# Performance work log

Measured on AMD Instinct MI355X. Metric: run time of the kernel, lower is better.

The kernel has to match this reference:

```python
import jax, jax.numpy as jnp
import numpy as np
import math

D_MODEL = 1024
MEM_SIZE = 4096
N_HEADS = 8
BATCH = 4
SEQ = 1024
TOP_K = min(SEQ, MEM_SIZE // 10)  # 409, matches torch: min(seq_len, memory_size//10)
UPDATE_RATE = 0.01


def _gelu(x):
    return jax.nn.gelu(x, approximate=False)  # torch nn.GELU default (erf)


def setup_inputs() -> dict:
    key = jax.random.key(0)
    ks = jax.random.split(key, 26)
    w = lambda k, shape, s=0.02: (jax.random.normal(k, shape, jnp.float32) * s)
    inp = {
        "x": jax.random.normal(ks[0], (BATCH, SEQ, D_MODEL), jnp.float32),
        "memory_bank": jax.random.normal(ks[1], (MEM_SIZE, D_MODEL), jnp.float32) * 0.1,
        "memory_indices": jax.random.randint(ks[2], (BATCH, TOP_K), 0, MEM_SIZE, jnp.int32),
        # memory_encoder: Linear -> GELU -> Linear
        "enc_w1": w(ks[3], (D_MODEL, D_MODEL)), "enc_b1": jnp.zeros((D_MODEL,), jnp.float32),
        "enc_w2": w(ks[4], (D_MODEL, D_MODEL)), "enc_b2": jnp.zeros((D_MODEL,), jnp.float32),
        # MultiheadAttention in/out projections
        "wq": w(ks[5], (D_MODEL, D_MODEL)), "bq": jnp.zeros((D_MODEL,), jnp.float32),
        "wk": w(ks[6], (D_MODEL, D_MODEL)), "bk": jnp.zeros((D_MODEL,), jnp.float32),
        "wv": w(ks[7], (D_MODEL, D_MODEL)), "bv": jnp.zeros((D_MODEL,), jnp.float32),
        "wo": w(ks[8], (D_MODEL, D_MODEL)), "bo": jnp.zeros((D_MODEL,), jnp.float32),
        # memory_decoder: Linear -> GELU -> Linear
        "dec_w1": w(ks[9], (D_MODEL, D_MODEL)), "dec_b1": jnp.zeros((D_MODEL,), jnp.float32),
        "dec_w2": w(ks[10], (D_MODEL, D_MODEL)), "dec_b2": jnp.zeros((D_MODEL,), jnp.float32),
        # LayerNorm
        "ln_g": jnp.ones((D_MODEL,), jnp.float32), "ln_b": jnp.zeros((D_MODEL,), jnp.float32),
        # importance_scorer: Linear(d,64) -> GELU -> Linear(64,1) -> Sigmoid
        "imp_w1": w(ks[11], (D_MODEL, 64)), "imp_b1": jnp.zeros((64,), jnp.float32),
        "imp_w2": w(ks[12], (64, 1)), "imp_b2": jnp.zeros((1,), jnp.float32),
    }
    return inp


def reference(x, memory_bank, memory_indices,
              enc_w1, enc_b1, enc_w2, enc_b2,
              wq, bq, wk, bk, wv, bv, wo, bo,
              dec_w1, dec_b1, dec_w2, dec_b2,
              ln_g, ln_b, imp_w1, imp_b1, imp_w2, imp_b2):
    B, L, D = x.shape
    M = memory_bank.shape[0]
    H = N_HEADS
    dh = D // H

    # memory_encoder (dropout inactive at eval)
    enc = _gelu(x @ enc_w1 + enc_b1) @ enc_w2 + enc_b2  # [B,L,D]

    # cross-attention: query = encoded input, key/value = memory bank (shared across batch)
    q = (enc @ wq + bq).reshape(B, L, H, dh)
    k = (memory_bank @ wk + bk).reshape(M, H, dh)
    v = (memory_bank @ wv + bv).reshape(M, H, dh)
    scores = jnp.einsum('blhd,mhd->bhlm', q, k) * (1.0 / math.sqrt(dh))
    attn = jax.nn.softmax(scores, axis=-1)                 # [B,H,L,M]
    ctx = jnp.einsum('bhlm,mhd->blhd', attn, v).reshape(B, L, D)
    mem_out = ctx @ wo + bo

    # memory_decoder + residual + LayerNorm
    dec = _gelu(mem_out @ dec_w1 + dec_b1) @ dec_w2 + dec_b2
    comb = x + dec
    mu = jnp.mean(comb, axis=-1, keepdims=True)
    var = jnp.var(comb, axis=-1, keepdims=True)
    out = (comb - mu) / jnp.sqrt(var + 1e-5) * ln_g + ln_b  # [B,L,D]

    # _update_memory: importance top-k select + sequential EMA scatter into memory bank
    imp = jax.nn.sigmoid(_gelu(x @ imp_w1 + imp_b1) @ imp_w2 + imp_b2)[..., 0]  # [B,L]
    _, top_idx = jax.lax.top_k(imp, TOP_K)                  # [B,K]
    top_tok = jnp.take_along_axis(x, top_idx[..., None], axis=1)  # [B,K,D]

    # faithful to the torch double loop (b outer, k inner): sequential EMA with
    # chained updates on index collisions
    flat_idx = memory_indices.reshape(-1)
    flat_tok = top_tok.reshape(-1, D)

    def body(mem, xs):
        i, t = xs
        row = (1.0 - UPDATE_RATE) * mem[i] + UPDATE_RATE * t
        return mem.at[i].set(row), None

    new_mem, _ = jax.lax.scan(body, memory_bank, (flat_idx, flat_tok))
    return out, new_mem
```

## Files before the change

### kernel.cpp

```cpp
#include <hip/hip_runtime.h>

typedef unsigned short u16;
typedef __attribute__((ext_vector_type(4))) int i4;
typedef __attribute__((ext_vector_type(4))) unsigned u4;
typedef __attribute__((ext_vector_type(4))) unsigned short us4;
typedef __attribute__((ext_vector_type(8))) short short8;
typedef __attribute__((ext_vector_type(4))) float f4;

#define D_MODEL 1024
#define ROWS 4096
#define NHEAD 8
#define DH 128
#define TOPK 409
#define NUPD 1636
#define NBATCH 4
#define MAXC 64
#define ATTNROWS 32768

__device__ __forceinline__ u16 f2bf(float f) {
  unsigned u = __builtin_bit_cast(unsigned, f);
  u += 0x7fffu + ((u >> 16) & 1u);
  return (u16)(u >> 16);
}
__device__ __forceinline__ float bf2f(u16 b) {
  unsigned u = ((unsigned)b) << 16;
  return __builtin_bit_cast(float, u);
}
__device__ __forceinline__ float gelu_f(float v) {
  return 0.5f * v * (1.0f + erff(v * 0.70710678118654752f));
}
__device__ __forceinline__ void gload16(const void* g, void* l) {
  __builtin_amdgcn_global_load_lds((const __attribute__((address_space(1))) void*)g,
                                   (__attribute__((address_space(3))) void*)l, 16, 0, 0);
}

__global__ __launch_bounds__(256) void conv_kernel(const float* __restrict__ in,
                                                   u16* __restrict__ out, int n4) {
  int i = blockIdx.x * 256 + threadIdx.x;
  if (i < n4) {
    f4 v = ((const f4*)in)[i];
    us4 o;
    o.x = f2bf(v.x); o.y = f2bf(v.y); o.z = f2bf(v.z); o.w = f2bf(v.w);
    ((us4*)out)[i] = o;
  }
}

__global__ __launch_bounds__(256) void wtrans8_kernel(const float* s0, const float* s1,
                                                      const float* s2, const float* s3,
                                                      const float* s4, const float* s5,
                                                      const float* s6, const float* s7,
                                                      u16* __restrict__ dst) {
  const float* srcs[8] = {s0, s1, s2, s3, s4, s5, s6, s7};
  const float* w = srcs[blockIdx.z];
  u16* wt = dst + (size_t)blockIdx.z * (1024 * 1024);
  __shared__ float t[32][33];
  int tx = threadIdx.x & 31, ty = threadIdx.x >> 5;
  int k0 = blockIdx.y * 32, n0 = blockIdx.x * 32;
  for (int r = 0; r < 4; ++r)
    t[ty + r * 8][tx] = w[(size_t)(k0 + ty + r * 8) * 1024 + n0 + tx];
  __syncthreads();
  for (int r = 0; r < 4; ++r)
    wt[(size_t)(n0 + ty + r * 8) * 1024 + k0 + tx] = f2bf(t[tx][ty + r * 8]);
}

template <int EPI>
__global__ __launch_bounds__(256) void gemm_bt(const u16* __restrict__ A,
                                               const u16* __restrict__ BT,
                                               const float* __restrict__ bias,
                                               void* __restrict__ C) {
  __shared__ __align__(16) char al[2 * 128 * 64];
  __shared__ __align__(16) char bl[2 * 64 * 64];
  const int K = 1024, N = 1024;
  const int id = blockIdx.x;
  const int xcd = id & 7, j = id >> 3;
  const int m0 = ((j & 3) * 8 + xcd) * 128;
  const int n0 = (j >> 2) * 64;
  const int tid = threadIdx.x;
  const int lane = tid & 63, wid = tid >> 6;
  const int g = lane >> 4, qi = lane & 15;
  const int wr = wid >> 1, wc = wid & 1;
  f4 acc[4][2] = {};

  const int a0r = tid >> 2, a0b = (tid & 3) ^ ((a0r >> 1) & 3);
  const int c1 = tid + 256;
  const int a1r = c1 >> 2, a1b = (c1 & 3) ^ ((a1r >> 1) & 3);
  const int b0r = tid >> 2, b0b = (tid & 3) ^ ((b0r >> 1) & 3);

#define STAGE(buf, kt)                                                                   \
  {                                                                                      \
    const int k0_ = (kt) * 32;                                                           \
    gload16(A + (size_t)(m0 + a0r) * K + k0_ + a0b * 8, al + (buf) * 8192 + tid * 16);   \
    gload16(A + (size_t)(m0 + a1r) * K + k0_ + a1b * 8, al + (buf) * 8192 + c1 * 16);    \
    gload16(BT + (size_t)(n0 + b0r) * K + k0_ + b0b * 8, bl + (buf) * 4096 + tid * 16);  \
  }

  STAGE(0, 0);
  __syncthreads();
  int cur = 0;
  for (int kt = 0; kt < 32; ++kt) {
    if (kt + 1 < 32) STAGE(cur ^ 1, kt + 1);
    short8 af[4], bfr[2];
    for (int i = 0; i < 4; ++i) {
      int r = wr * 64 + i * 16 + qi;
      af[i] = *(const short8*)(al + cur * 8192 + r * 64 + ((g ^ ((r >> 1) & 3))) * 16);
    }
    for (int sn = 0; sn < 2; ++sn) {
      int r = wc * 32 + sn * 16 + qi;
      bfr[sn] = *(const short8*)(bl + cur * 4096 + r * 64 + ((g ^ ((r >> 1) & 3))) * 16);
    }
    for (int i = 0; i < 4; ++i)
      for (int sn = 0; sn < 2; ++sn)
        acc[i][sn] = __builtin_amdgcn_mfma_f32_16x16x32_bf16(af[i], bfr[sn], acc[i][sn], 0, 0, 0);
    __syncthreads();
    cur ^= 1;
  }
#undef STAGE

  for (int i = 0; i < 4; ++i) {
    int row = m0 + wr * 64 + i * 16 + g * 4;
    for (int sn = 0; sn < 2; ++sn) {
      int col = n0 + wc * 32 + sn * 16 + qi;
      float bv = bias[col];
      for (int jj = 0; jj < 4; ++jj) {
        float v = acc[i][sn][jj] + bv;
        if constexpr (EPI == 1) v = gelu_f(v);
        if constexpr (EPI == 2)
          ((float*)C)[(size_t)(row + jj) * N + col] = v;
        else
          ((u16*)C)[(size_t)(row + jj) * N + col] = f2bf(v);
      }
    }
  }
}

__global__ __launch_bounds__(256) void gemm_kv(const u16* __restrict__ A,
                                               const u16* __restrict__ BT,
                                               const float* __restrict__ bk,
                                               const float* __restrict__ bv,
                                               u16* __restrict__ Ck, u16* __restrict__ CvT) {
  __shared__ __align__(16) char pool[2 * 128 * 64 + 2 * 64 * 64];
  char* al = pool;
  char* bl = pool + 2 * 128 * 64;
  const int id = blockIdx.x;
  const int xcd = id & 7, j = id >> 3;
  const int m0 = ((j & 3) * 8 + xcd) * 128;
  const int n0 = (j >> 2) * 64;
  const int tid = threadIdx.x;
  const int lane = tid & 63, wid = tid >> 6;
  const int g = lane >> 4, qi = lane & 15;
  const int wr = wid >> 1, wc = wid & 1;
  const int K = 1024, M = 4096;
  f4 acc[4][2] = {};

  const int a0r = tid >> 2, a0b = (tid & 3) ^ ((a0r >> 1) & 3);
  const int c1 = tid + 256;
  const int a1r = c1 >> 2, a1b = (c1 & 3) ^ ((a1r >> 1) & 3);
  const int b0r = tid >> 2, b0b = (tid & 3) ^ ((b0r >> 1) & 3);

#define STAGE(buf, kt)                                                                   \
  {                                                                                      \
    const int k0_ = (kt) * 32;                                                           \
    gload16(A + (size_t)(m0 + a0r) * K + k0_ + a0b * 8, al + (buf) * 8192 + tid * 16);   \
    gload16(A + (size_t)(m0 + a1r) * K + k0_ + a1b * 8, al + (buf) * 8192 + c1 * 16);    \
    gload16(BT + (size_t)(n0 + b0r) * K + k0_ + b0b * 8, bl + (buf) * 4096 + tid * 16);  \
  }

  STAGE(0, 0);
  __syncthreads();
  int cur = 0;
  for (int kt = 0; kt < 32; ++kt) {
    if (kt + 1 < 32) STAGE(cur ^ 1, kt + 1);
    short8 af[4], bfr[2];
    for (int i = 0; i < 4; ++i) {
      int r = wr * 64 + i * 16 + qi;
      af[i] = *(const short8*)(al + cur * 8192 + r * 64 + ((g ^ ((r >> 1) & 3))) * 16);
    }
    for (int sn = 0; sn < 2; ++sn) {
      int r = wc * 32 + sn * 16 + qi;
      bfr[sn] = *(const short8*)(bl + cur * 4096 + r * 64 + ((g ^ ((r >> 1) & 3))) * 16);
    }
    for (int i = 0; i < 4; ++i)
      for (int sn = 0; sn < 2; ++sn)
        acc[i][sn] = __builtin_amdgcn_mfma_f32_16x16x32_bf16(af[i], bfr[sn], acc[i][sn], 0, 0, 0);
    __syncthreads();
    cur ^= 1;
  }
#undef STAGE

  if (n0 < 1024) {
    for (int i = 0; i < 4; ++i) {
      int row = m0 + wr * 64 + i * 16 + g * 4;
      for (int sn = 0; sn < 2; ++sn) {
        int col = n0 + wc * 32 + sn * 16 + qi;
        float bvv = bk[col];
        for (int jj = 0; jj < 4; ++jj)
          Ck[(size_t)(row + jj) * 1024 + col] = f2bf(acc[i][sn][jj] + bvv);
      }
    }
  } else {
    u16(*t)[132] = (u16(*)[132])pool;
    __syncthreads();
    for (int i = 0; i < 4; ++i)
      for (int sn = 0; sn < 2; ++sn) {
        int nl = wc * 32 + sn * 16 + qi;
        float bvv = bv[n0 - 1024 + nl];
        for (int jj = 0; jj < 4; ++jj)
          t[nl][wr * 64 + i * 16 + g * 4 + jj] = f2bf(acc[i][sn][jj] + bvv);
      }
    __syncthreads();
    int r = tid >> 2, cg = tid & 3;
    for (int v = 0; v < 4; ++v) {
      us4 val = *(const us4*)&t[r][cg * 32 + v * 8];
      *(us4*)&CvT[(size_t)(n0 - 1024 + r) * M + m0 + cg * 32 + v * 8] = val;
    }
  }
}

template <int LP>
__global__ __launch_bounds__(512) void attn_kernel(const u16* __restrict__ q,
                                                   const u16* __restrict__ kp,
                                                   const u16* __restrict__ vT,
                                                   u16* __restrict__ cp0, u16* __restrict__ cp1,
                                                   u16* __restrict__ cp2, u16* __restrict__ cp3,
                                                   float* __restrict__ ml) {
  constexpr int MR = 4096 >> LP;
  constexpr int NT = MR / 64;
  __shared__ __align__(16) char kl[64 * 256];
  __shared__ __align__(16) char vl[128 * 128];
  const int id = blockIdx.x;
  const int h = id & 7;
  const int rest = id >> 3;
  const int part = rest & ((1 << LP) - 1);
  const int qblk = (rest >> LP) & 7;
  const int b = rest >> (3 + LP);
  const int tid = threadIdx.x;
  const int lane = tid & 63, wid = tid >> 6;
  const int g = lane >> 4, qi = lane & 15;
  const int qrow = b * 1024 + qblk * 128 + wid * 16 + qi;
  const float scale = 0.08838834764831845f;
  u16* ctp = (part == 0) ? cp0 : (part == 1) ? cp1 : (part == 2) ? cp2 : cp3;

  short8 qf[4];
  for (int kk = 0; kk < 4; ++kk)
    qf[kk] = *(const short8*)(q + (size_t)qrow * 1024 + h * 128 + kk * 32 + g * 8);

  const int kc0 = tid, kc1 = tid + 512;
  const int kr0 = kc0 >> 4, kb0 = kc0 & 15, kr1 = kc1 >> 4, kb1 = kc1 & 15;
  const int vr0 = kc0 >> 3, vb0 = kc0 & 7, vr1 = kc1 >> 3, vb1 = kc1 & 7;
  const int kd0 = kr0 * 256 + (kb0 ^ (kr0 & 7)) * 16;
  const int kd1 = kr1 * 256 + (kb1 ^ (kr1 & 7)) * 16;
  const int vd0 = vr0 * 128 + (vb0 ^ (vr0 & 7)) * 16;
  const int vd1 = vr1 * 128 + (vb1 ^ (vr1 & 7)) * 16;
  const int mbase = part * MR;
  const u16* kg0 = kp + (size_t)kr0 * 1024 + h * 128 + kb0 * 8;
  const u16* kg1 = kp + (size_t)kr1 * 1024 + h * 128 + kb1 * 8;
  const u16* vg0 = vT + (size_t)(h * 128 + vr0) * 4096 + vb0 * 8;
  const u16* vg1 = vT + (size_t)(h * 128 + vr1) * 4096 + vb1 * 8;

  i4 kreg0, kreg1, vreg0, vreg1;
#define LOADREGS(mt_)                                  \
  {                                                    \
    const int m0_ = mbase + (mt_) * 64;                \
    kreg0 = *(const i4*)(kg0 + (size_t)m0_ * 1024);    \
    kreg1 = *(const i4*)(kg1 + (size_t)m0_ * 1024);    \
    vreg0 = *(const i4*)(vg0 + m0_);                   \
    vreg1 = *(const i4*)(vg1 + m0_);                   \
  }

  f4 ct[8] = {};
  float mrun = -1e30f, lsum = 0.0f;

  LOADREGS(0);
  for (int mt = 0; mt < NT; ++mt) {
    __syncthreads();
    *(i4*)(kl + kd0) = kreg0;
    *(i4*)(kl + kd1) = kreg1;
    *(i4*)(vl + vd0) = vreg0;
    *(i4*)(vl + vd1) = vreg1;
    __syncthreads();
    if (mt + 1 < NT) LOADREGS(mt + 1);

    f4 st[4] = {};
    for (int s = 0; s < 4; ++s) {
      int n = s * 16 + qi;
      const char* krow = kl + n * 256;
      int sw = n & 7;
      for (int kk = 0; kk < 4; ++kk) {
        short8 a = *(const short8*)(krow + ((kk * 4 + g) ^ sw) * 16);
        st[s] = __builtin_amdgcn_mfma_f32_16x16x32_bf16(a, qf[kk], st[s], 0, 0, 0);
      }
    }
    float sv[16];
    float tmax = -1e30f;
    for (int s = 0; s < 4; ++s)
      for (int jj = 0; jj < 4; ++jj) {
        float v = st[s][jj] * scale;
        sv[s * 4 + jj] = v;
        tmax = fmaxf(tmax, v);
      }
    tmax = fmaxf(tmax, __shfl_xor(tmax, 16, 64));
    tmax = fmaxf(tmax, __shfl_xor(tmax, 32, 64));
    float mnew = fmaxf(mrun, tmax);
    float r = __expf(mrun - mnew);
    float psum = 0.0f;
    for (int i = 0; i < 16; ++i) {
      sv[i] = __expf(sv[i] - mnew);
      psum += sv[i];
    }
    psum += __shfl_xor(psum, 16, 64);
    psum += __shfl_xor(psum, 32, 64);
    lsum = lsum * r + psum;
    mrun = mnew;
    for (int i = 0; i < 8; ++i) ct[i] = ct[i] * r;

    unsigned pk0[4], pk1[4];
    for (int s = 0; s < 4; ++s) {
      pk0[s] = (unsigned)f2bf(sv[s * 4 + 0]) | ((unsigned)f2bf(sv[s * 4 + 1]) << 16);
      pk1[s] = (unsigned)f2bf(sv[s * 4 + 2]) | ((unsigned)f2bf(sv[s * 4 + 3]) << 16);
    }
    const int src1 = qi + ((g & 1) << 5);
    const int src2 = src1 + 16;
    const bool hi = (g & 2) != 0;
    for (int p = 0; p < 2; ++p) {
      unsigned a0 = __shfl(pk0[2 * p], src1, 64), b0 = __shfl(pk0[2 * p + 1], src1, 64);
      unsigned a1 = __shfl(pk1[2 * p], src1, 64), b1 = __shfl(pk1[2 * p + 1], src1, 64);
      unsigned a2 = __shfl(pk0[2 * p], src2, 64), b2 = __shfl(pk0[2 * p + 1], src2, 64);
      unsigned a3 = __shfl(pk1[2 * p], src2, 64), b3 = __shfl(pk1[2 * p + 1], src2, 64);
      u4 bw;
      bw.x = hi ? b0 : a0; bw.y = hi ? b1 : a1; bw.z = hi ? b2 : a2; bw.w = hi ? b3 : a3;
      short8 pf = __builtin_bit_cast(short8, bw);
      for (int d = 0; d < 8; ++d) {
        int dr = d * 16 + qi;
        short8 a = *(const short8*)(vl + dr * 128 + (((p * 4 + g) ^ (dr & 7))) * 16);
        ct[d] = __builtin_amdgcn_mfma_f32_16x16x32_bf16(a, pf, ct[d], 0, 0, 0);
      }
    }
  }
#undef LOADREGS

  const int orow = ((b * 8 + h) << 10) + qblk * 128 + wid * 16 + qi;
  if (g == 0) {
    ml[(size_t)(part * ATTNROWS + orow) * 2 + 0] = mrun;
    ml[(size_t)(part * ATTNROWS + orow) * 2 + 1] = lsum;
  }
  for (int d = 0; d < 8; ++d) {
    us4 o;
    o.x = f2bf(ct[d][0]); o.y = f2bf(ct[d][1]);
    o.z = f2bf(ct[d][2]); o.w = f2bf(ct[d][3]);
    *(us4*)(ctp + (size_t)orow * 128 + d * 16 + g * 4) = o;
  }
}

__global__ __launch_bounds__(256) void combine4_kernel(const u16* __restrict__ cp0,
                                                       const u16* __restrict__ cp1,
                                                       const u16* __restrict__ cp2,
                                                       const u16* __restrict__ cp3,
                                                       const float* __restrict__ ml,
                                                       u16* __restrict__ ctx) {
  int tid = threadIdx.x;
  int row = blockIdx.x * 16 + (tid >> 4);
  int dp = (tid & 15) * 8;
  float m0 = ml[(size_t)row * 2], l0 = ml[(size_t)row * 2 + 1];
  float m1 = ml[((size_t)ATTNROWS + row) * 2], l1 = ml[((size_t)ATTNROWS + row) * 2 + 1];
  float m2 = ml[((size_t)2 * ATTNROWS + row) * 2], l2 = ml[((size_t)2 * ATTNROWS + row) * 2 + 1];
  float m3 = ml[((size_t)3 * ATTNROWS + row) * 2], l3 = ml[((size_t)3 * ATTNROWS + row) * 2 + 1];
  float m = fmaxf(fmaxf(m0, m1), fmaxf(m2, m3));
  float s0 = __expf(m0 - m), s1 = __expf(m1 - m), s2 = __expf(m2 - m), s3 = __expf(m3 - m);
  float inv = 1.0f / (l0 * s0 + l1 * s1 + l2 * s2 + l3 * s3);
  short8 c0 = *(const short8*)(cp0 + (size_t)row * 128 + dp);
  short8 c1 = *(const short8*)(cp1 + (size_t)row * 128 + dp);
  short8 c2 = *(const short8*)(cp2 + (size_t)row * 128 + dp);
  short8 c3 = *(const short8*)(cp3 + (size_t)row * 128 + dp);
  us4 o[2];
  for (int i = 0; i < 8; ++i) {
    float f = (bf2f((u16)c0[i]) * s0 + bf2f((u16)c1[i]) * s1 + bf2f((u16)c2[i]) * s2 +
               bf2f((u16)c3[i]) * s3) * inv;
    ((u16*)o)[i] = f2bf(f);
  }
  int bb = row >> 13, hh = (row >> 10) & 7, qr = row & 1023;
  *(short8*)(ctx + (size_t)((bb << 10) + qr) * 1024 + hh * 128 + dp) =
      __builtin_bit_cast(short8, o);
}

__global__ __launch_bounds__(256) void ln_kernel(const float* __restrict__ x,
                                                 const float* __restrict__ dec,
                                                 const float* __restrict__ gw,
                                                 const float* __restrict__ bw,
                                                 float* __restrict__ out,
                                                 int* __restrict__ cnt) {
  __shared__ float rs[256], rs2[256];
  int row = blockIdx.x, tid = threadIdx.x;
  if (tid == 0) cnt[row] = 0;
  float c[4];
  float s = 0.0f, s2 = 0.0f;
  for (int i = 0; i < 4; ++i) {
    int col = tid + i * 256;
    float v = x[(size_t)row * 1024 + col] + dec[(size_t)row * 1024 + col];
    c[i] = v; s += v; s2 += v * v;
  }
  rs[tid] = s; rs2[tid] = s2;
  __syncthreads();
  for (int st = 128; st > 0; st >>= 1) {
    if (tid < st) { rs[tid] += rs[tid + st]; rs2[tid] += rs2[tid + st]; }
    __syncthreads();
  }
  float mu = rs[0] * (1.0f / 1024.0f);
  float var = rs2[0] * (1.0f / 1024.0f) - mu * mu;
  float inv = rsqrtf(var + 1e-5f);
  for (int i = 0; i < 4; ++i) {
    int col = tid + i * 256;
    out[(size_t)row * 1024 + col] = (c[i] - mu) * inv * gw[col] + bw[col];
  }
}

__global__ __launch_bounds__(256) void imp_kernel(const float* __restrict__ x,
                                                  const float* __restrict__ w1,
                                                  const float* __restrict__ b1,
                                                  const float* __restrict__ w2,
                                                  const float* __restrict__ b2,
                                                  float* __restrict__ imp) {
  __shared__ float xs[8][1024];
  int tid = threadIdx.x;
  int lane = tid & 63, wid = tid >> 6;
  size_t base = (size_t)blockIdx.x * 8192;
  for (int i = 0; i < 32; ++i) ((float*)xs)[tid + i * 256] = x[base + tid + i * 256];
  __syncthreads();
  int r0 = wid * 2, r1 = wid * 2 + 1;
  float a0 = 0.0f, a1 = 0.0f;
  for (int k = 0; k < 1024; ++k) {
    float wv = w1[k * 64 + lane];
    a0 += xs[r0][k] * wv;
    a1 += xs[r1][k] * wv;
  }
  float h0 = gelu_f(a0 + b1[lane]) * w2[lane];
  float h1 = gelu_f(a1 + b1[lane]) * w2[lane];
  for (int d = 1; d < 64; d <<= 1) {
    h0 += __shfl_xor(h0, d, 64);
    h1 += __shfl_xor(h1, d, 64);
  }
  if (lane == 0) {
    imp[blockIdx.x * 8 + r0] = 1.0f / (1.0f + expf(-(h0 + b2[0])));
    imp[blockIdx.x * 8 + r1] = 1.0f / (1.0f + expf(-(h1 + b2[0])));
  }
}

__global__ __launch_bounds__(512) void topk_kernel(const float* __restrict__ imp,
                                                   int* __restrict__ tidx) {
  __shared__ float v[1024];
  __shared__ int ix[1024];
  int b = blockIdx.x, tid = threadIdx.x;
  for (int i = tid; i < 1024; i += 512) { v[i] = imp[b * 1024 + i]; ix[i] = i; }
  __syncthreads();
  for (int k = 2; k <= 1024; k <<= 1) {
    for (int j = k >> 1; j > 0; j >>= 1) {
      for (int t = tid; t < 1024; t += 512) {
        int p = t ^ j;
        if (p > t) {
          float va = v[t], vb = v[p];
          int ia = ix[t], ib = ix[p];
          bool ord = (va > vb) || (va == vb && ia < ib);
          bool up = ((t & k) == 0);
          if (up ? !ord : ord) { v[t] = vb; v[p] = va; ix[t] = ib; ix[p] = ia; }
        }
      }
      __syncthreads();
    }
  }
  for (int t = tid; t < TOPK; t += 512) tidx[b * TOPK + t] = ix[t];
}

__global__ __launch_bounds__(128) void rank_kernel(const int* __restrict__ midx,
                                                   int* __restrict__ cnt,
                                                   int* __restrict__ slot) {
  __shared__ int mi[NUPD];
  int tid = threadIdx.x;
  for (int i = tid; i < NUPD; i += 128) mi[i] = midx[i];
  __syncthreads();
  int j = blockIdx.x * 128 + tid;
  if (j < NUPD) {
    int r = mi[j], rank = 0;
    for (int jp = 0; jp < j; ++jp) rank += (mi[jp] == r) ? 1 : 0;
    if (rank < MAXC) slot[r * MAXC + rank] = j;
    atomicAdd(&cnt[r], 1);
  }
}

__global__ __launch_bounds__(256) void apply_kernel(const float* __restrict__ x,
                                                    const float* __restrict__ mem,
                                                    const int* __restrict__ tidx,
                                                    const int* __restrict__ cnt,
                                                    const int* __restrict__ slot,
                                                    float* __restrict__ outm) {
  int row = blockIdx.x, tid = threadIdx.x;
  f4 acc = ((const f4*)(mem + (size_t)row * 1024))[tid];
  int c = cnt[row];
  c = c < MAXC ? c : MAXC;
  for (int t = 0; t < c; ++t) {
    int j = slot[row * MAXC + t];
    int b = j / TOPK;
    int tr = tidx[j];
    f4 xv = ((const f4*)(x + ((size_t)b * 1024 + tr) * 1024))[tid];
    acc = acc * 0.99f + xv * 0.01f;
  }
  ((f4*)(outm + (size_t)row * 1024))[tid] = acc;
}

extern "C" void kernel_launch(void* const* d_in, const int* in_sizes, int n_in,
                              void* d_out, int out_size, void* d_ws, size_t ws_size,
                              hipStream_t stream) {
  const float* x = (const float*)d_in[0];
  const float* memory_bank = (const float*)d_in[1];
  const int* memory_indices = (const int*)d_in[2];
  const float* enc_w1 = (const float*)d_in[3];
  const float* enc_b1 = (const float*)d_in[4];
  const float* enc_w2 = (const float*)d_in[5];
  const float* enc_b2 = (const float*)d_in[6];
  const float* wq = (const float*)d_in[7];
  const float* bq = (const float*)d_in[8];
  const float* wk = (const float*)d_in[9];
  const float* bk = (const float*)d_in[10];
  const float* wv = (const float*)d_in[11];
  const float* bv = (const float*)d_in[12];
  const float* wo = (const float*)d_in[13];
  const float* bo = (const float*)d_in[14];
  const float* dec_w1 = (const float*)d_in[15];
  const float* dec_b1 = (const float*)d_in[16];
  const float* dec_w2 = (const float*)d_in[17];
  const float* dec_b2 = (const float*)d_in[18];
  const float* ln_g = (const float*)d_in[19];
  const float* ln_b = (const float*)d_in[20];
  const float* imp_w1 = (const float*)d_in[21];
  const float* imp_b1 = (const float*)d_in[22];
  const float* imp_w2 = (const float*)d_in[23];
  const float* imp_b2 = (const float*)d_in[24];

  char* ws = (char*)d_ws;
  u16* buf0 = (u16*)(ws);
  u16* buf1 = (u16*)(ws + (8ull << 20));
  u16* buf2 = (u16*)(ws + (16ull << 20));
  u16* buf3 = (u16*)(ws + (24ull << 20));
  u16* buf4 = (u16*)(ws + (32ull << 20));
  float* decb = (float*)(ws + (40ull << 20));
  u16* wtb = (u16*)(ws + (56ull << 20));
  float* impb = (float*)(ws + (72ull << 20));
  int* tidx = (int*)(ws + (72ull << 20) + (1 << 16));
  int* cnt = (int*)buf3;
  int* slot = (int*)(ws + (24ull << 20) + (1 << 16));
  u16* cp0 = buf0;
  u16* cp1 = buf2;
  u16* cp2 = (u16*)(ws + (40ull << 20));
  u16* cp3 = (u16*)(ws + (48ull << 20));
  float* ml = (float*)(ws + (56ull << 20));

  const int NM = 1024 * 1024;
  u16* wt_e1 = wtb + 0 * NM;
  u16* wt_e2 = wtb + 1 * NM;
  u16* wt_q = wtb + 2 * NM;
  u16* wt_k = wtb + 3 * NM;
  u16* wt_o = wtb + 5 * NM;
  u16* wt_d1 = wtb + 6 * NM;
  u16* wt_d2 = wtb + 7 * NM;

  conv_kernel<<<4096, 256, 0, stream>>>(x, buf0, ROWS * D_MODEL / 4);
  conv_kernel<<<4096, 256, 0, stream>>>(memory_bank, buf2, ROWS * D_MODEL / 4);
  wtrans8_kernel<<<dim3(32, 32, 8), 256, 0, stream>>>(enc_w1, enc_w2, wq, wk, wv, wo,
                                                      dec_w1, dec_w2, wtb);

  gemm_bt<1><<<512, 256, 0, stream>>>(buf0, wt_e1, enc_b1, buf1);
  gemm_bt<0><<<512, 256, 0, stream>>>(buf1, wt_e2, enc_b2, buf0);
  gemm_bt<0><<<512, 256, 0, stream>>>(buf0, wt_q, bq, buf1);
  gemm_kv<<<1024, 256, 0, stream>>>(buf2, wt_k, bk, bv, buf3, buf4);

  attn_kernel<2><<<1024, 512, 0, stream>>>(buf1, buf3, buf4, cp0, cp1, cp2, cp3, ml);
  combine4_kernel<<<2048, 256, 0, stream>>>(cp0, cp1, cp2, cp3, ml, buf1);

  gemm_bt<0><<<512, 256, 0, stream>>>(buf1, wt_o, bo, buf0);
  gemm_bt<1><<<512, 256, 0, stream>>>(buf0, wt_d1, dec_b1, buf2);
  gemm_bt<2><<<512, 256, 0, stream>>>(buf2, wt_d2, dec_b2, decb);
  ln_kernel<<<4096, 256, 0, stream>>>(x, decb, ln_g, ln_b, (float*)d_out, cnt);

  imp_kernel<<<512, 256, 0, stream>>>(x, imp_w1, imp_b1, imp_w2, imp_b2, impb);
  topk_kernel<<<NBATCH, 512, 0, stream>>>(impb, tidx);
  rank_kernel<<<13, 128, 0, stream>>>(memory_indices, cnt, slot);
  apply_kernel<<<4096, 256, 0, stream>>>(x, memory_bank, tidx, cnt, slot,
                                         (float*)d_out + (size_t)ROWS * D_MODEL);
}
```

Before: 442.2 us.

## Process two query tiles per wave in attention to reuse K/V fragments

```diff
diff --git a/kernel.cpp b/kernel.cpp
--- a/kernel.cpp
+++ b/kernel.cpp
@@ -217,12 +217,12 @@
 }
 
 template <int LP>
-__global__ __launch_bounds__(512) void attn_kernel(const u16* __restrict__ q,
-                                                   const u16* __restrict__ kp,
-                                                   const u16* __restrict__ vT,
-                                                   u16* __restrict__ cp0, u16* __restrict__ cp1,
-                                                   u16* __restrict__ cp2, u16* __restrict__ cp3,
-                                                   float* __restrict__ ml) {
+__global__ __launch_bounds__(256, 3) void attn_kernel(const u16* __restrict__ q,
+                                                      const u16* __restrict__ kp,
+                                                      const u16* __restrict__ vT,
+                                                      u16* __restrict__ cp0, u16* __restrict__ cp1,
+                                                      u16* __restrict__ cp2, u16* __restrict__ cp3,
+                                                      float* __restrict__ ml) {
   constexpr int MR = 4096 >> LP;
   constexpr int NT = MR / 64;
   __shared__ __align__(16) char kl[64 * 256];
@@ -236,118 +236,171 @@
   const int tid = threadIdx.x;
   const int lane = tid & 63, wid = tid >> 6;
   const int g = lane >> 4, qi = lane & 15;
-  const int qrow = b * 1024 + qblk * 128 + wid * 16 + qi;
+  const int qrow0 = b * 1024 + qblk * 128 + wid * 32 + qi;
+  const int qrow1 = qrow0 + 16;
   const float scale = 0.08838834764831845f;
   u16* ctp = (part == 0) ? cp0 : (part == 1) ? cp1 : (part == 2) ? cp2 : cp3;
 
-  short8 qf[4];
-  for (int kk = 0; kk < 4; ++kk)
-    qf[kk] = *(const short8*)(q + (size_t)qrow * 1024 + h * 128 + kk * 32 + g * 8);
-
-  const int kc0 = tid, kc1 = tid + 512;
+  short8 qf0[4], qf1[4];
+  for (int kk = 0; kk < 4; ++kk) {
+    qf0[kk] = *(const short8*)(q + (size_t)qrow0 * 1024 + h * 128 + kk * 32 + g * 8);
+    qf1[kk] = *(const short8*)(q + (size_t)qrow1 * 1024 + h * 128 + kk * 32 + g * 8);
+  }
+
+  const int kc0 = tid, kc1 = tid + 256, kc2 = tid + 512, kc3 = tid + 768;
   const int kr0 = kc0 >> 4, kb0 = kc0 & 15, kr1 = kc1 >> 4, kb1 = kc1 & 15;
+  const int kr2 = kc2 >> 4, kb2 = kc2 & 15, kr3 = kc3 >> 4, kb3 = kc3 & 15;
   const int vr0 = kc0 >> 3, vb0 = kc0 & 7, vr1 = kc1 >> 3, vb1 = kc1 & 7;
+  const int vr2 = kc2 >> 3, vb2 = kc2 & 7, vr3 = kc3 >> 3, vb3 = kc3 & 7;
   const int kd0 = kr0 * 256 + (kb0 ^ (kr0 & 7)) * 16;
   const int kd1 = kr1 * 256 + (kb1 ^ (kr1 & 7)) * 16;
+  const int kd2 = kr2 * 256 + (kb2 ^ (kr2 & 7)) * 16;
+  const int kd3 = kr3 * 256 + (kb3 ^ (kr3 & 7)) * 16;
   const int vd0 = vr0 * 128 + (vb0 ^ (vr0 & 7)) * 16;
   const int vd1 = vr1 * 128 + (vb1 ^ (vr1 & 7)) * 16;
+  const int vd2 = vr2 * 128 + (vb2 ^ (vr2 & 7)) * 16;
+  const int vd3 = vr3 * 128 + (vb3 ^ (vr3 & 7)) * 16;
   const int mbase = part * MR;
-  const u16* kg0 = kp + (size_t)kr0 * 1024 + h * 128 + kb0 * 8;
-  const u16* kg1 = kp + (size_t)kr1 * 1024 + h * 128 + kb1 * 8;
-  const u16* vg0 = vT + (size_t)(h * 128 + vr0) * 4096 + vb0 * 8;
-  const u16* vg1 = vT + (size_t)(h * 128 + vr1) * 4096 + vb1 * 8;
-
-  i4 kreg0, kreg1, vreg0, vreg1;
-#define LOADREGS(mt_)                                  \
-  {                                                    \
-    const int m0_ = mbase + (mt_) * 64;                \
-    kreg0 = *(const i4*)(kg0 + (size_t)m0_ * 1024);    \
-    kreg1 = *(const i4*)(kg1 + (size_t)m0_ * 1024);    \
-    vreg0 = *(const i4*)(vg0 + m0_);                   \
-    vreg1 = *(const i4*)(vg1 + m0_);                   \
-  }
-
-  f4 ct[8] = {};
-  float mrun = -1e30f, lsum = 0.0f;
-
-  LOADREGS(0);
+  const u16* kg0 = kp + (size_t)(mbase + kr0) * 1024 + h * 128 + kb0 * 8;
+  const u16* kg1 = kp + (size_t)(mbase + kr1) * 1024 + h * 128 + kb1 * 8;
+  const u16* kg2 = kp + (size_t)(mbase + kr2) * 1024 + h * 128 + kb2 * 8;
+  const u16* kg3 = kp + (size_t)(mbase + kr3) * 1024 + h * 128 + kb3 * 8;
+  const u16* vg0 = vT + (size_t)(h * 128 + vr0) * 4096 + mbase + vb0 * 8;
+  const u16* vg1 = vT + (size_t)(h * 128 + vr1) * 4096 + mbase + vb1 * 8;
+  const u16* vg2 = vT + (size_t)(h * 128 + vr2) * 4096 + mbase + vb2 * 8;
+  const u16* vg3 = vT + (size_t)(h * 128 + vr3) * 4096 + mbase + vb3 * 8;
+
+  i4 kreg0, kreg1, kreg2, kreg3, vreg0, vreg1, vreg2, vreg3;
+#define LOADK()                                             \
+  {                                                         \
+    kreg0 = *(const i4*)kg0; kg0 += 64 * 1024;              \
+    kreg1 = *(const i4*)kg1; kg1 += 64 * 1024;              \
+    kreg2 = *(const i4*)kg2; kg2 += 64 * 1024;              \
+    kreg3 = *(const i4*)kg3; kg3 += 64 * 1024;              \
+  }
+#define LOADV()                                             \
+  {                                                         \
+    vreg0 = *(const i4*)vg0; vg0 += 64;                     \
+    vreg1 = *(const i4*)vg1; vg1 += 64;                     \
+    vreg2 = *(const i4*)vg2; vg2 += 64;                     \
+    vreg3 = *(const i4*)vg3; vg3 += 64;                     \
+  }
+
+  f4 ct0[8] = {}, ct1[8] = {};
+  float mrun0 = -1e30f, lsum0 = 0.0f, mrun1 = -1e30f, lsum1 = 0.0f;
+
+  LOADK();
+  LOADV();
   for (int mt = 0; mt < NT; ++mt) {
     __syncthreads();
-    *(i4*)(kl + kd0) = kreg0;
-    *(i4*)(kl + kd1) = kreg1;
-    *(i4*)(vl + vd0) = vreg0;
-    *(i4*)(vl + vd1) = vreg1;
+    *(i4*)(kl + kd0) = kreg0; *(i4*)(kl + kd1) = kreg1;
+    *(i4*)(kl + kd2) = kreg2; *(i4*)(kl + kd3) = kreg3;
+    *(i4*)(vl + vd0) = vreg0; *(i4*)(vl + vd1) = vreg1;
+    *(i4*)(vl + vd2) = vreg2; *(i4*)(vl + vd3) = vreg3;
     __syncthreads();
-    if (mt + 1 < NT) LOADREGS(mt + 1);
-
-    f4 st[4] = {};
+    const bool more = (mt + 1 < NT);
+    if (more) LOADK();
+
+    f4 st0[4] = {}, st1[4] = {};
     for (int s = 0; s < 4; ++s) {
       int n = s * 16 + qi;
       const char* krow = kl + n * 256;
       int sw = n & 7;
       for (int kk = 0; kk < 4; ++kk) {
         short8 a = *(const short8*)(krow + ((kk * 4 + g) ^ sw) * 16);
-        st[s] = __builtin_amdgcn_mfma_f32_16x16x32_bf16(a, qf[kk], st[s], 0, 0, 0);
+        st0[s] = __builtin_amdgcn_mfma_f32_16x16x32_bf16(a, qf0[kk], st0[s], 0, 0, 0);
+        st1[s] = __builtin_amdgcn_mfma_f32_16x16x32_bf16(a, qf1[kk], st1[s], 0, 0, 0);
       }
     }
-    float sv[16];
-    float tmax = -1e30f;
-    for (int s = 0; s < 4; ++s)
-      for (int jj = 0; jj < 4; ++jj) {
-        float v = st[s][jj] * scale;
-        sv[s * 4 + jj] = v;
-        tmax = fmaxf(tmax, v);
-      }
-    tmax = fmaxf(tmax, __shfl_xor(tmax, 16, 64));
-    tmax = fmaxf(tmax, __shfl_xor(tmax, 32, 64));
-    float mnew = fmaxf(mrun, tmax);
-    float r = __expf(mrun - mnew);
-    float psum = 0.0f;
-    for (int i = 0; i < 16; ++i) {
-      sv[i] = __expf(sv[i] - mnew);
-      psum += sv[i];
-    }
-    psum += __shfl_xor(psum, 16, 64);
-    psum += __shfl_xor(psum, 32, 64);
-    lsum = lsum * r + psum;
-    mrun = mnew;
-    for (int i = 0; i < 8; ++i) ct[i] = ct[i] * r;
-
-    unsigned pk0[4], pk1[4];
-    for (int s = 0; s < 4; ++s) {
-      pk0[s] = (unsigned)f2bf(sv[s * 4 + 0]) | ((unsigned)f2bf(sv[s * 4 + 1]) << 16);
-      pk1[s] = (unsigned)f2bf(sv[s * 4 + 2]) | ((unsigned)f2bf(sv[s * 4 + 3]) << 16);
-    }
-    const int src1 = qi + ((g & 1) << 5);
-    const int src2 = src1 + 16;
-    const bool hi = (g & 2) != 0;
-    for (int p = 0; p < 2; ++p) {
-      unsigned a0 = __shfl(pk0[2 * p], src1, 64), b0 = __shfl(pk0[2 * p + 1], src1, 64);
-      unsigned a1 = __shfl(pk1[2 * p], src1, 64), b1 = __shfl(pk1[2 * p + 1], src1, 64);
-      unsigned a2 = __shfl(pk0[2 * p], src2, 64), b2 = __shfl(pk0[2 * p + 1], src2, 64);
-      unsigned a3 = __shfl(pk1[2 * p], src2, 64), b3 = __shfl(pk1[2 * p + 1], src2, 64);
-      u4 bw;
-      bw.x = hi ? b0 : a0; bw.y = hi ? b1 : a1; bw.z = hi ? b2 : a2; bw.w = hi ? b3 : a3;
-      short8 pf = __builtin_bit_cast(short8, bw);
-      for (int d = 0; d < 8; ++d) {
-        int dr = d * 16 + qi;
-        short8 a = *(const short8*)(vl + dr * 128 + (((p * 4 + g) ^ (dr & 7))) * 16);
-        ct[d] = __builtin_amdgcn_mfma_f32_16x16x32_bf16(a, pf, ct[d], 0, 0, 0);
-      }
-    }
-  }
-#undef LOADREGS
-
-  const int orow = ((b * 8 + h) << 10) + qblk * 128 + wid * 16 + qi;
+
+    short8 pfa0, pfb0, pfa1, pfb1;
+#define SOFTMAX_PACK(ST, MRUN, LSUM, CT, PFA, PFB)                                        \
+    {                                                                                     \
+      float sv[16];                                                                       \
+      float tmax = -1e30f;                                                                \
+      for (int s = 0; s < 4; ++s)                                                         \
+        for (int jj = 0; jj < 4; ++jj) {                                                  \
+          float v = ST[s][jj] * scale;                                                    \
+          sv[s * 4 + jj] = v;                                                             \
+          tmax = fmaxf(tmax, v);                                                          \
+        }                                                                                 \
+      tmax = fmaxf(tmax, __shfl_xor(tmax, 16, 64));                                       \
+      tmax = fmaxf(tmax, __shfl_xor(tmax, 32, 64));                                       \
+      float mnew = fmaxf(MRUN, tmax);                                                     \
+      float r = __expf(MRUN - mnew);                                                      \
+      float psum = 0.0f;                                                                  \
+      for (int i = 0; i < 16; ++i) {                                                      \
+        sv[i] = __expf(sv[i] - mnew);                                                     \
+        psum += sv[i];                                                                    \
+      }                                                                                   \
+      psum += __shfl_xor(psum, 16, 64);                                                   \
+      psum += __shfl_xor(psum, 32, 64);                                                   \
+      LSUM = LSUM * r + psum;                                                             \
+      MRUN = mnew;                                                                        \
+      for (int i = 0; i < 8; ++i) CT[i] = CT[i] * r;                                      \
+      unsigned pk0[4], pk1[4];                                                            \
+      for (int s = 0; s < 4; ++s) {                                                       \
+        pk0[s] = (unsigned)f2bf(sv[s * 4 + 0]) | ((unsigned)f2bf(sv[s * 4 + 1]) << 16);   \
+        pk1[s] = (unsigned)f2bf(sv[s * 4 + 2]) | ((unsigned)f2bf(sv[s * 4 + 3]) << 16);   \
+      }                                                                                   \
+      const int src1 = qi + ((g & 1) << 5);                                               \
+      const int src2 = src1 + 16;                                                         \
+      const bool hi = (g & 2) != 0;                                                       \
+      {                                                                                   \
+        unsigned a0 = __shfl(pk0[0], src1, 64), b0 = __shfl(pk0[1], src1, 64);            \
+        unsigned a1 = __shfl(pk1[0], src1, 64), b1 = __shfl(pk1[1], src1, 64);            \
+        unsigned a2 = __shfl(pk0[0], src2, 64), b2 = __shfl(pk0[1], src2, 64);            \
+        unsigned a3 = __shfl(pk1[0], src2, 64), b3 = __shfl(pk1[1], src2, 64);            \
+        u4 bw;                                                                            \
+        bw.x = hi ? b0 : a0; bw.y = hi ? b1 : a1; bw.z = hi ? b2 : a2; bw.w = hi ? b3 : a3;\
+        PFA = __builtin_bit_cast(short8, bw);                                             \
+      }                                                                                   \
+      {                                                                                   \
+        unsigned a0 = __shfl(pk0[2], src1, 64), b0 = __shfl(pk0[3], src1, 64);            \
+        unsigned a1 = __shfl(pk1[2], src1, 64), b1 = __shfl(pk1[3], src1, 64);            \
+        unsigned a2 = __shfl(pk0[2], src2, 64), b2 = __shfl(pk0[3], src2, 64);            \
+        unsigned a3 = __shfl(pk1[2], src2, 64), b3 = __shfl(pk1[3], src2, 64);            \
+        u4 bw;                                                                            \
+        bw.x = hi ? b0 : a0; bw.y = hi ? b1 : a1; bw.z = hi ? b2 : a2; bw.w = hi ? b3 : a3;\
+        PFB = __builtin_bit_cast(short8, bw);                                             \
+      }                                                                                   \
+    }
+    SOFTMAX_PACK(st0, mrun0, lsum0, ct0, pfa0, pfb0);
+    SOFTMAX_PACK(st1, mrun1, lsum1, ct1, pfa1, pfb1);
+#undef SOFTMAX_PACK
+
+    if (more) LOADV();
+
+    for (int d = 0; d < 8; ++d) {
+      int dr = d * 16 + qi;
+      const char* vrow = vl + dr * 128;
+      int swv = dr & 7;
+      short8 a0 = *(const short8*)(vrow + ((0 * 4 + g) ^ swv) * 16);
+      ct0[d] = __builtin_amdgcn_mfma_f32_16x16x32_bf16(a0, pfa0, ct0[d], 0, 0, 0);
+      ct1[d] = __builtin_amdgcn_mfma_f32_16x16x32_bf16(a0, pfa1, ct1[d], 0, 0, 0);
+      short8 a1 = *(const short8*)(vrow + ((1 * 4 + g) ^ swv) * 16);
+      ct0[d] = __builtin_amdgcn_mfma_f32_16x16x32_bf16(a1, pfb0, ct0[d], 0, 0, 0);
+      ct1[d] = __builtin_amdgcn_mfma_f32_16x16x32_bf16(a1, pfb1, ct1[d], 0, 0, 0);
+    }
+  }
+#undef LOADK
+#undef LOADV
+
+  const int obase = ((b * 8 + h) << 10) + qblk * 128 + wid * 32 + qi;
   if (g == 0) {
-    ml[(size_t)(part * ATTNROWS + orow) * 2 + 0] = mrun;
-    ml[(size_t)(part * ATTNROWS + orow) * 2 + 1] = lsum;
+    ml[(size_t)(part * ATTNROWS + obase) * 2 + 0] = mrun0;
+    ml[(size_t)(part * ATTNROWS + obase) * 2 + 1] = lsum0;
+    ml[(size_t)(part * ATTNROWS + obase + 16) * 2 + 0] = mrun1;
+    ml[(size_t)(part * ATTNROWS + obase + 16) * 2 + 1] = lsum1;
   }
   for (int d = 0; d < 8; ++d) {
-    us4 o;
-    o.x = f2bf(ct[d][0]); o.y = f2bf(ct[d][1]);
-    o.z = f2bf(ct[d][2]); o.w = f2bf(ct[d][3]);
-    *(us4*)(ctp + (size_t)orow * 128 + d * 16 + g * 4) = o;
+    us4 o0, o1;
+    o0.x = f2bf(ct0[d][0]); o0.y = f2bf(ct0[d][1]);
+    o0.z = f2bf(ct0[d][2]); o0.w = f2bf(ct0[d][3]);
+    o1.x = f2bf(ct1[d][0]); o1.y = f2bf(ct1[d][1]);
+    o1.z = f2bf(ct1[d][2]); o1.w = f2bf(ct1[d][3]);
+    *(us4*)(ctp + (size_t)obase * 128 + d * 16 + g * 4) = o0;
+    *(us4*)(ctp + (size_t)(obase + 16) * 128 + d * 16 + g * 4) = o1;
   }
 }
 
@@ -571,7 +624,7 @@
   gemm_bt<0><<<512, 256, 0, stream>>>(buf0, wt_q, bq, buf1);
   gemm_kv<<<1024, 256, 0, stream>>>(buf2, wt_k, bk, bv, buf3, buf4);
 
-  attn_kernel<2><<<1024, 512, 0, stream>>>(buf1, buf3, buf4, cp0, cp1, cp2, cp3, ml);
+  attn_kernel<2><<<1024, 256, 0, stream>>>(buf1, buf3, buf4, cp0, cp1, cp2, cp3, ml);
   combine4_kernel<<<2048, 256, 0, stream>>>(cp0, cp1, cp2, cp3, ml, buf1);
 
   gemm_bt<0><<<512, 256, 0, stream>>>(buf1, wt_o, bo, buf0);
```

Result: slower. 632.9 us (+43.1%).

## Fold consecutive linear layers (enc_w2·wq, wo·dec_w1) into precomputed weight products

Applied to the files above, without the earlier changes.

```diff
diff --git a/kernel.cpp b/kernel.cpp
--- a/kernel.cpp
+++ b/kernel.cpp
@@ -61,6 +61,91 @@
   __syncthreads();
   for (int r = 0; r < 4; ++r)
     wt[(size_t)(n0 + ty + r * 8) * 1024 + k0 + tx] = f2bf(t[tx][ty + r * 8]);
+}
+
+__global__ __launch_bounds__(256) void bias_prep_kernel(const float* __restrict__ b2,
+                                                        const float* __restrict__ wq,
+                                                        const float* __restrict__ bq,
+                                                        const float* __restrict__ bo,
+                                                        const float* __restrict__ dw1,
+                                                        const float* __restrict__ db1,
+                                                        float* __restrict__ bqp,
+                                                        float* __restrict__ bodp) {
+  int id = blockIdx.x;
+  int n = (id & 3) * 256 + threadIdx.x;
+  const float* bvec = (id < 4) ? b2 : bo;
+  const float* W = (id < 4) ? wq : dw1;
+  const float* badd = (id < 4) ? bq : db1;
+  float* out = (id < 4) ? bqp : bodp;
+  float s = 0.0f;
+  for (int k = 0; k < 1024; ++k) s += bvec[k] * W[(size_t)k * 1024 + n];
+  out[n] = s + badd[n];
+}
+
+__global__ __launch_bounds__(256) void gemm_sq(const u16* __restrict__ A0,
+                                               const u16* __restrict__ B0,
+                                               u16* __restrict__ C0,
+                                               const u16* __restrict__ A1,
+                                               const u16* __restrict__ B1,
+                                               u16* __restrict__ C1) {
+  __shared__ __align__(16) char al[2 * 128 * 64];
+  __shared__ __align__(16) char bl[2 * 64 * 64];
+  const int K = 1024, N = 1024;
+  const int id = blockIdx.x;
+  const int which = id >> 7, j = id & 127;
+  const u16* A = which ? A1 : A0;
+  const u16* BT = which ? B1 : B0;
+  u16* C = which ? C1 : C0;
+  const int m0 = (j >> 4) * 128, n0 = (j & 15) * 64;
+  const int tid = threadIdx.x;
+  const int lane = tid & 63, wid = tid >> 6;
+  const int g = lane >> 4, qi = lane & 15;
+  const int wr = wid >> 1, wc = wid & 1;
+  f4 acc[4][2] = {};
+
+  const int a0r = tid >> 2, a0b = (tid & 3) ^ ((a0r >> 1) & 3);
+  const int c1 = tid + 256;
+  const int a1r = c1 >> 2, a1b = (c1 & 3) ^ ((a1r >> 1) & 3);
+  const int b0r = tid >> 2, b0b = (tid & 3) ^ ((b0r >> 1) & 3);
+
+#define STAGE(buf, kt)                                                                   \
+  {                                                                                      \
+    const int k0_ = (kt) * 32;                                                           \
+    gload16(A + (size_t)(m0 + a0r) * K + k0_ + a0b * 8, al + (buf) * 8192 + tid * 16);   \
+    gload16(A + (size_t)(m0 + a1r) * K + k0_ + a1b * 8, al + (buf) * 8192 + c1 * 16);    \
+    gload16(BT + (size_t)(n0 + b0r) * K + k0_ + b0b * 8, bl + (buf) * 4096 + tid * 16);  \
+  }
+
+  STAGE(0, 0);
+  __syncthreads();
+  int cur = 0;
+  for (int kt = 0; kt < 32; ++kt) {
+    if (kt + 1 < 32) STAGE(cur ^ 1, kt + 1);
+    short8 af[4], bfr[2];
+    for (int i = 0; i < 4; ++i) {
+      int r = wr * 64 + i * 16 + qi;
+      af[i] = *(const short8*)(al + cur * 8192 + r * 64 + ((g ^ ((r >> 1) & 3))) * 16);
+    }
+    for (int sn = 0; sn < 2; ++sn) {
+      int r = wc * 32 + sn * 16 + qi;
+      bfr[sn] = *(const short8*)(bl + cur * 4096 + r * 64 + ((g ^ ((r >> 1) & 3))) * 16);
+    }
+    for (int i = 0; i < 4; ++i)
+      for (int sn = 0; sn < 2; ++sn)
+        acc[i][sn] = __builtin_amdgcn_mfma_f32_16x16x32_bf16(af[i], bfr[sn], acc[i][sn], 0, 0, 0);
+    __syncthreads();
+    cur ^= 1;
+  }
+#undef STAGE
+
+  for (int i = 0; i < 4; ++i) {
+    int row = m0 + wr * 64 + i * 16 + g * 4;
+    for (int sn = 0; sn < 2; ++sn) {
+      int col = n0 + wc * 32 + sn * 16 + qi;
+      for (int jj = 0; jj < 4; ++jj)
+        C[(size_t)(row + jj) * N + col] = f2bf(acc[i][sn][jj]);
+    }
+  }
 }
 
 template <int EPI>
@@ -544,9 +629,13 @@
   u16* wtb = (u16*)(ws + (56ull << 20));
   float* impb = (float*)(ws + (72ull << 20));
   int* tidx = (int*)(ws + (72ull << 20) + (1 << 16));
+  float* bqp = (float*)(ws + (72ull << 20) + (1 << 17));
+  float* bodp = (float*)(ws + (72ull << 20) + (1 << 17) + 4096);
   int* cnt = (int*)buf3;
   int* slot = (int*)(ws + (24ull << 20) + (1 << 16));
-  u16* cp0 = buf0;
+  u16* w2n = (u16*)(ws + (40ull << 20));
+  u16* won = (u16*)(ws + (42ull << 20));
+  u16* cp0 = buf1;
   u16* cp1 = buf2;
   u16* cp2 = (u16*)(ws + (40ull << 20));
   u16* cp3 = (u16*)(ws + (48ull << 20));
@@ -554,10 +643,10 @@
 
   const int NM = 1024 * 1024;
   u16* wt_e1 = wtb + 0 * NM;
-  u16* wt_e2 = wtb + 1 * NM;
+  u16* wt_e2q = wtb + 1 * NM;
   u16* wt_q = wtb + 2 * NM;
   u16* wt_k = wtb + 3 * NM;
-  u16* wt_o = wtb + 5 * NM;
+  u16* wt_od = wtb + 5 * NM;
   u16* wt_d1 = wtb + 6 * NM;
   u16* wt_d2 = wtb + 7 * NM;
 
@@ -565,18 +654,21 @@
   conv_kernel<<<4096, 256, 0, stream>>>(memory_bank, buf2, ROWS * D_MODEL / 4);
   wtrans8_kernel<<<dim3(32, 32, 8), 256, 0, stream>>>(enc_w1, enc_w2, wq, wk, wv, wo,
                                                       dec_w1, dec_w2, wtb);
+  conv_kernel<<<1024, 256, 0, stream>>>(enc_w2, w2n, NM / 4);
+  conv_kernel<<<1024, 256, 0, stream>>>(wo, won, NM / 4);
+
+  gemm_sq<<<256, 256, 0, stream>>>(wt_q, w2n, wt_e2q, wt_d1, won, wt_od);
+  bias_prep_kernel<<<8, 256, 0, stream>>>(enc_b2, wq, bq, bo, dec_w1, dec_b1, bqp, bodp);
 
   gemm_bt<1><<<512, 256, 0, stream>>>(buf0, wt_e1, enc_b1, buf1);
-  gemm_bt<0><<<512, 256, 0, stream>>>(buf1, wt_e2, enc_b2, buf0);
-  gemm_bt<0><<<512, 256, 0, stream>>>(buf0, wt_q, bq, buf1);
+  gemm_bt<0><<<512, 256, 0, stream>>>(buf1, wt_e2q, bqp, buf0);
   gemm_kv<<<1024, 256, 0, stream>>>(buf2, wt_k, bk, bv, buf3, buf4);
 
-  attn_kernel<2><<<1024, 512, 0, stream>>>(buf1, buf3, buf4, cp0, cp1, cp2, cp3, ml);
-  combine4_kernel<<<2048, 256, 0, stream>>>(cp0, cp1, cp2, cp3, ml, buf1);
-
-  gemm_bt<0><<<512, 256, 0, stream>>>(buf1, wt_o, bo, buf0);
-  gemm_bt<1><<<512, 256, 0, stream>>>(buf0, wt_d1, dec_b1, buf2);
-  gemm_bt<2><<<512, 256, 0, stream>>>(buf2, wt_d2, dec_b2, decb);
+  attn_kernel<2><<<1024, 512, 0, stream>>>(buf0, buf3, buf4, cp0, cp1, cp2, cp3, ml);
+  combine4_kernel<<<2048, 256, 0, stream>>>(cp0, cp1, cp2, cp3, ml, buf0);
+
+  gemm_bt<1><<<512, 256, 0, stream>>>(buf0, wt_od, bodp, buf1);
+  gemm_bt<2><<<512, 256, 0, stream>>>(buf1, wt_d2, dec_b2, decb);
   ln_kernel<<<4096, 256, 0, stream>>>(x, decb, ln_g, ln_b, (float*)d_out, cnt);
 
   imp_kernel<<<512, 256, 0, stream>>>(x, imp_w1, imp_b1, imp_w2, imp_b2, impb);
```

New measurement: 455.2 us. +2.9%, slower.
